# Optimization experiments

Measured on AMD Instinct MI355X. Metric: run time of the kernel, lower is better.

Reference implementation:

```python
import jax, jax.numpy as jnp
import numpy as np

N = 10000
E = 160000
IN_C = 512
OUT_C = 1024
NEG_SLOPE = 0.2


def setup_inputs() -> dict:
    key = jax.random.key(0)
    ks = jax.random.split(key, 12)
    x = jax.random.normal(ks[0], (N, IN_C), dtype=jnp.float32)
    edge_index = jax.random.randint(ks[1], (2, E), 0, N, dtype=jnp.int32)
    s_in = 1.0 / np.sqrt(IN_C)
    s_out = 1.0 / np.sqrt(OUT_C)
    return {
        "x": x,
        "edge_index": edge_index,
        "W1": jax.random.normal(ks[2], (IN_C, OUT_C), dtype=jnp.float32) * s_in,
        "a_src1": jax.random.normal(ks[3], (OUT_C,), dtype=jnp.float32) * s_out,
        "a_dst1": jax.random.normal(ks[4], (OUT_C,), dtype=jnp.float32) * s_out,
        "b1": jnp.zeros((OUT_C,), dtype=jnp.float32),
        "W2": jax.random.normal(ks[5], (IN_C, OUT_C), dtype=jnp.float32) * s_in,
        "a_src2": jax.random.normal(ks[6], (OUT_C,), dtype=jnp.float32) * s_out,
        "a_dst2": jax.random.normal(ks[7], (OUT_C,), dtype=jnp.float32) * s_out,
        "b2": jnp.zeros((OUT_C,), dtype=jnp.float32),
        "prelu_a": jnp.asarray(0.25, dtype=jnp.float32),
        "Wp1": jax.random.normal(ks[8], (OUT_C, OUT_C), dtype=jnp.float32) * s_out,
        "bp1": jnp.zeros((OUT_C,), dtype=jnp.float32),
        "Wp2": jax.random.normal(ks[9], (OUT_C, 1024), dtype=jnp.float32) * s_out,
    }


def _gat_conv(x, src, dst, W, a_src, a_dst, b):
    # x: [N, in], W: [in, out]. PyG GATConv, heads=1, self-loops already in src/dst.
    h = x @ W  # [N, out]
    alpha_s = h @ a_src  # [N]
    alpha_d = h @ a_dst  # [N]
    e = alpha_s[src] + alpha_d[dst]  # [E+N]
    e = jnp.where(e >= 0, e, NEG_SLOPE * e)  # LeakyReLU(0.2)
    # segment softmax over destination nodes
    m = jax.ops.segment_max(e, dst, num_segments=N)  # [N]
    ex = jnp.exp(e - m[dst])
    denom = jax.ops.segment_sum(ex, dst, num_segments=N)  # [N], >=1 via self-loops
    alpha = ex / denom[dst]  # [E+N]
    out = jax.ops.segment_sum(alpha[:, None] * h[src], dst, num_segments=N)
    return out + b


def reference(x, edge_index, W1, a_src1, a_dst1, b1, W2, a_src2, a_dst2, b2,
              prelu_a, Wp1, bp1, Wp2):
    # add self loops (PyG GATConv default)
    loops = jnp.arange(N, dtype=edge_index.dtype)
    src = jnp.concatenate([edge_index[0], loops])
    dst = jnp.concatenate([edge_index[1], loops])

    def prelu(v):
        return jnp.where(v >= 0, v, prelu_a * v)

    h1 = prelu(_gat_conv(x, src, dst, W1, a_src1, a_dst1, b1))  # [N, 1024]
    h2 = prelu(_gat_conv(x, src, dst, W2, a_src2, a_dst2, b2))  # [N, 1024]
    h = h1 + h2

    # semantic attention: project -> mean over nodes -> softmax over 1024 dims
    w = jnp.tanh(h @ Wp1 + bp1) @ Wp2  # [N, 1024]
    w = w.mean(axis=0)  # [1024]
    att = jax.nn.softmax(w, axis=0)  # [1024] == beta.mean(0).squeeze()
    return att * h1 + (1.0 - att) * h2
```

## Files before the change

### kernel.cpp

```cpp
#include <hip/hip_runtime.h>

#define IN_C 512
#define OUT_C 1024
#define NC2 2048
#define NEG_SLOPE 0.2f

typedef short frag8 __attribute__((ext_vector_type(8)));
typedef float f32x4 __attribute__((ext_vector_type(4)));

#define GLOAD_LDS16(g, l) __builtin_amdgcn_global_load_lds(\
    (const __attribute__((address_space(1))) void*)(g), \
    (__attribute__((address_space(3))) void*)(l), 16, 0, 0)

__device__ __forceinline__ unsigned short f2b(float f){
  unsigned u = __float_as_uint(f);
  unsigned r = (u + 0x7fffu + ((u >> 16) & 1u)) >> 16;
  return (unsigned short)r;
}
__device__ __forceinline__ unsigned encf(float f){
  unsigned u = __float_as_uint(f);
  return (u & 0x80000000u) ? ~u : (u | 0x80000000u);
}
__device__ __forceinline__ float decf(unsigned u){
  unsigned v = (u & 0x80000000u) ? (u & 0x7fffffffu) : ~u;
  return __uint_as_float(v);
}
__device__ __forceinline__ float leaky(float v){ return v >= 0.f ? v : NEG_SLOPE * v; }


__global__ void prep_kernel(const float* __restrict__ W1, const float* __restrict__ W2,
                            const float* __restrict__ Wp1,
                            const float* __restrict__ a_src1, const float* __restrict__ a_dst1,
                            const float* __restrict__ a_src2, const float* __restrict__ a_dst2,
                            unsigned short* __restrict__ WT, unsigned short* __restrict__ Wp1T,
                            float* __restrict__ uv){
  __shared__ float tile[32][33];
  int b = blockIdx.x;
  int tx = threadIdx.x & 31, ty = threadIdx.x >> 5;
  if (b < 1024){
    const float* in = (b >> 9) ? W2 : W1;
    int rowOff = (b >> 9) * OUT_C;
    int bb = b & 511;
    int c0 = (bb & 31) * 32, r0 = (bb >> 5) * 32;
    for (int i = ty; i < 32; i += 8)
      tile[i][tx] = in[(size_t)(r0 + i) * OUT_C + c0 + tx];
    __syncthreads();
    for (int i = ty; i < 32; i += 8)
      WT[(size_t)(c0 + i + rowOff) * IN_C + r0 + tx] = f2b(tile[tx][i]);
  } else if (b < 2048){
    int bb = b - 1024;
    int c0 = (bb & 31) * 32, r0 = (bb >> 5) * 32;
    for (int i = ty; i < 32; i += 8)
      tile[i][tx] = Wp1[(size_t)(r0 + i) * OUT_C + c0 + tx];
    __syncthreads();
    for (int i = ty; i < 32; i += 8)
      Wp1T[(size_t)(c0 + i) * OUT_C + r0 + tx] = f2b(tile[tx][i]);
  } else {
    int g = (b - 2048) * 4 + (threadIdx.x >> 6);
    int lane = threadIdx.x & 63;
    int which = g >> 9;
    int i = g & 511;
    const float* W = (which < 2) ? W1 : W2;
    const float* a = (which == 0) ? a_src1 : (which == 1) ? a_dst1 : (which == 2) ? a_src2 : a_dst2;
    const float* row = W + (size_t)i * OUT_C;
    float s = 0.f;
    for (int j = lane; j < OUT_C; j += 64) s += row[j] * a[j];
    for (int off = 32; off; off >>= 1) s += __shfl_down(s, off);
    if (lane == 0) uv[which * IN_C + i] = s;
  }
}


__global__ void alpha_kernel(const float* __restrict__ x, const float* __restrict__ uv,
                             unsigned short* __restrict__ xb,
                             float* __restrict__ as1, float* __restrict__ ad1,
                             float* __restrict__ as2, float* __restrict__ ad2,
                             float* __restrict__ self1, float* __restrict__ self2,
                             unsigned* __restrict__ m1e, unsigned* __restrict__ m2e,
                             int* counts, int* cursor, float* colsum, float* wv){
  int n = blockIdx.x;
  int w = threadIdx.x >> 6, lane = threadIdx.x & 63;
  __shared__ float sh[4];
  if (threadIdx.x == 0){ counts[n] = 0; cursor[n] = 0; }
  if (n < 8){
    int i = n * 256 + threadIdx.x;
    if (i < 1024) colsum[i] = 0.f; else wv[i - 1024] = 0.f;
  }
  const float* row = x + (size_t)n * IN_C;
  const float* u = uv + w * IN_C;
  float s = 0.f;
  for (int j = lane; j < IN_C; j += 64){
    float v = row[j];
    s += v * u[j];
    if (w == 0) xb[(size_t)n * IN_C + j] = f2b(v);
  }
  for (int off = 32; off; off >>= 1) s += __shfl_down(s, off);
  if (lane == 0){
    sh[w] = s;
    if (w == 0) as1[n] = s;
    else if (w == 1) ad1[n] = s;
    else if (w == 2) as2[n] = s;
    else ad2[n] = s;
  }
  __syncthreads();
  if (threadIdx.x == 0){
    float e1 = leaky(sh[0] + sh[1]);
    float e2 = leaky(sh[2] + sh[3]);
    self1[n] = e1; self2[n] = e2;
    m1e[n] = encf(e1); m2e[n] = encf(e2);
  }
}


__global__ void histmax_kernel(const int* __restrict__ src, const int* __restrict__ dst,
                               const float* __restrict__ as1, const float* __restrict__ ad1,
                               const float* __restrict__ as2, const float* __restrict__ ad2,
                               int* counts, unsigned* m1e, unsigned* m2e, int E){
  int e = blockIdx.x * 256 + threadIdx.x;
  if (e >= E) return;
  int s = src[e], d = dst[e];
  atomicAdd(&counts[d], 1);
  atomicMax(&m1e[d], encf(leaky(as1[s] + ad1[d])));
  atomicMax(&m2e[d], encf(leaky(as2[s] + ad2[d])));
}

__global__ void scanA_kernel(const int* __restrict__ counts, int* __restrict__ offs,
                             int* __restrict__ bsum, int n){
  __shared__ int wsum[4];
  int i = blockIdx.x * 256 + threadIdx.x;
  int wave = threadIdx.x >> 6, lane = threadIdx.x & 63;
  int v = (i < n) ? counts[i] : 0;
  int sc = v;
  for (int o = 1; o < 64; o <<= 1){
    int t = __shfl_up(sc, o);
    if (lane >= o) sc += t;
  }
  if (lane == 63) wsum[wave] = sc;
  __syncthreads();
  int wp = 0, tot = 0;
#pragma unroll
  for (int k = 0; k < 4; k++){
    int ws = wsum[k];
    if (k < wave) wp += ws;
    tot += ws;
  }
  if (i < n) offs[i] = wp + sc - v;
  if (threadIdx.x == 0) bsum[blockIdx.x] = tot;
}

__global__ void scanB_kernel(int* __restrict__ bsum, int nb){
  int lane = threadIdx.x;
  int v = (lane < nb) ? bsum[lane] : 0;
  int sc = v;
  for (int o = 1; o < 64; o <<= 1){
    int t = __shfl_up(sc, o);
    if (lane >= o) sc += t;
  }
  if (lane < nb) bsum[lane] = sc - v;
}

__global__ void scanC_kernel(int* __restrict__ offs, const int* __restrict__ bsum, int n){
  int i = blockIdx.x * 256 + threadIdx.x;
  if (i < n) offs[i] += bsum[blockIdx.x];
}

__global__ void denominit_kernel(const unsigned* __restrict__ m1e, const unsigned* __restrict__ m2e,
                                 const float* __restrict__ self1, const float* __restrict__ self2,
                                 float* __restrict__ m1, float* __restrict__ m2,
                                 float* __restrict__ den1, float* __restrict__ den2, int N){
  int i = blockIdx.x * 256 + threadIdx.x;
  if (i >= N) return;
  float a = decf(m1e[i]), b = decf(m2e[i]);
  m1[i] = a; m2[i] = b;
  den1[i] = expf(self1[i] - a);
  den2[i] = expf(self2[i] - b);
}

__global__ void scatterexp_kernel(const int* __restrict__ src, const int* __restrict__ dst,
                                  const int* __restrict__ offs, int* cursor,
                                  const float* __restrict__ as1, const float* __restrict__ ad1,
                                  const float* __restrict__ as2, const float* __restrict__ ad2,
                                  const float* __restrict__ m1, const float* __restrict__ m2,
                                  int* __restrict__ nsrc, float* __restrict__ nw1, float* __restrict__ nw2,
                                  float* den1, float* den2, int E){
  int e = blockIdx.x * 256 + threadIdx.x;
  if (e >= E) return;
  int s = src[e], d = dst[e];
  int p = atomicAdd(&cursor[d], 1);
  int idx = offs[d] + p;
  float x1 = expf(leaky(as1[s] + ad1[d]) - m1[d]);
  float x2 = expf(leaky(as2[s] + ad2[d]) - m2[d]);
  nsrc[idx] = s; nw1[idx] = x1; nw2[idx] = x2;
  atomicAdd(&den1[d], x1);
  atomicAdd(&den2[d], x2);
}


#define AGG_FMA8(ACC, W, U) \
  ACC[0] += (W) * __uint_as_float(((unsigned)(U).x) << 16); \
  ACC[1] += (W) * __uint_as_float(((unsigned)(U).x) & 0xffff0000u); \
  ACC[2] += (W) * __uint_as_float(((unsigned)(U).y) << 16); \
  ACC[3] += (W) * __uint_as_float(((unsigned)(U).y) & 0xffff0000u); \
  ACC[4] += (W) * __uint_as_float(((unsigned)(U).z) << 16); \
  ACC[5] += (W) * __uint_as_float(((unsigned)(U).z) & 0xffff0000u); \
  ACC[6] += (W) * __uint_as_float(((unsigned)(U).w) << 16); \
  ACC[7] += (W) * __uint_as_float(((unsigned)(U).w) & 0xffff0000u);

__global__ __launch_bounds__(256) void aggx_kernel(
    const int* __restrict__ counts, const int* __restrict__ offs,
    const int* __restrict__ nsrc, const float* __restrict__ nw1, const float* __restrict__ nw2,
    const float* __restrict__ den1, const float* __restrict__ den2,
    const float* __restrict__ self1, const float* __restrict__ self2,
    const float* __restrict__ m1, const float* __restrict__ m2,
    const unsigned short* __restrict__ xb,
    unsigned short* __restrict__ xa1b, unsigned short* __restrict__ xa2b, int N){
  int tid = threadIdx.x;
  int g = tid >> 4, hl = tid & 15;
  int grpbase = tid & 48;
  int d = blockIdx.y * 16 + g;
  if (d >= N) return;
  int colbase = blockIdx.x * 128 + hl * 8;
  float inv1 = 1.f / den1[d], inv2 = 1.f / den2[d];
  int deg = counts[d], off = offs[d];
  float acc1[8] = {0,0,0,0,0,0,0,0}, acc2[8] = {0,0,0,0,0,0,0,0};
  const unsigned short* Xb = xb + colbase;
  for (int base = 0; base < deg; base += 16){
    int i = base + hl;
    int s = 0; float w1 = 0.f, w2 = 0.f;
    if (i < deg){
      int p = off + i;
      s = nsrc[p];
      w1 = nw1[p] * inv1;
      w2 = nw2[p] * inv2;
    }
    int cnt = min(16, deg - base);
#pragma unroll 4
    for (int j = 0; j < cnt; j++){
      int sj = __shfl(s, grpbase + j);
      float w1j = __shfl(w1, grpbase + j);
      float w2j = __shfl(w2, grpbase + j);
      int4 u = *(const int4*)(Xb + (size_t)sj * IN_C);
      AGG_FMA8(acc1, w1j, u)
      AGG_FMA8(acc2, w2j, u)
    }
  }
  {
    float ws1 = expf(self1[d] - m1[d]) * inv1;
    float ws2 = expf(self2[d] - m2[d]) * inv2;
    int4 u = *(const int4*)(Xb + (size_t)d * IN_C);
    AGG_FMA8(acc1, ws1, u)
    AGG_FMA8(acc2, ws2, u)
  }
  size_t outb = (size_t)d * IN_C + colbase;
  int4 o1, o2;
  o1.x = (int)((unsigned)f2b(acc1[0]) | ((unsigned)f2b(acc1[1]) << 16));
  o1.y = (int)((unsigned)f2b(acc1[2]) | ((unsigned)f2b(acc1[3]) << 16));
  o1.z = (int)((unsigned)f2b(acc1[4]) | ((unsigned)f2b(acc1[5]) << 16));
  o1.w = (int)((unsigned)f2b(acc1[6]) | ((unsigned)f2b(acc1[7]) << 16));
  o2.x = (int)((unsigned)f2b(acc2[0]) | ((unsigned)f2b(acc2[1]) << 16));
  o2.y = (int)((unsigned)f2b(acc2[2]) | ((unsigned)f2b(acc2[3]) << 16));
  o2.z = (int)((unsigned)f2b(acc2[4]) | ((unsigned)f2b(acc2[5]) << 16));
  o2.w = (int)((unsigned)f2b(acc2[6]) | ((unsigned)f2b(acc2[7]) << 16));
  *(int4*)(xa1b + outb) = o1;
  *(int4*)(xa2b + outb) = o2;
}


__global__ __launch_bounds__(256) void gemmh_kernel(const unsigned short* __restrict__ A1,
                                                    const unsigned short* __restrict__ A2,
                                                    const unsigned short* __restrict__ BT,
                                                    const float* __restrict__ b1,
                                                    const float* __restrict__ b2,
                                                    const float* __restrict__ prelu_a,
                                                    unsigned short* __restrict__ hsum,
                                                    unsigned short* __restrict__ hdiff,
                                                    int M, int Mtiles, int perx){
  const int bid = blockIdx.x;
  const int xcd = bid & 7;
  const int li = bid >> 3;
  const int bn_t = li & 7;
  const int bm_t = xcd * perx + (li >> 3);
  if (bm_t >= Mtiles) return;
  const int bm = bm_t * 64, bn = bn_t * 128;
  __shared__ unsigned short Al[64 * 32];
  __shared__ unsigned short Bl[128 * 32];
  const int t = threadIdx.x;
  const int lane = t & 63, wid = t >> 6;
  const int wj = wid;
  const int l16 = lane & 15, q = lane >> 4;
  const int lch = (lane & 3) * 8;
  f32x4 acc1[4][2] = {};
  f32x4 acc2[4][2] = {};
  const int arow = bm + wid * 16 + (lane >> 2);
  const int brow0 = bn + wid * 32 + (lane >> 2);
  const int ga = min(arow, M - 1);
  const unsigned short* pa1 = A1 + (size_t)ga * IN_C + lch;
  const unsigned short* pa2 = A2 + (size_t)ga * IN_C + lch;
  const unsigned short* pb0 = BT + (size_t)brow0 * IN_C + lch;
  const unsigned short* pb1 = BT + (size_t)(brow0 + 16) * IN_C + lch;
  const size_t boff2 = (size_t)OUT_C * IN_C;
  for (int k0 = 0; k0 < IN_C; k0 += 32){
    GLOAD_LDS16(pa1 + k0, &Al[(wid * 16) * 32]);
    GLOAD_LDS16(pb0 + k0, &Bl[(wid * 32) * 32]);
    GLOAD_LDS16(pb1 + k0, &Bl[(wid * 32 + 16) * 32]);
    __syncthreads();
    frag8 af[4], bf[2];
#pragma unroll
    for (int mi = 0; mi < 4; mi++) af[mi] = *(const frag8*)&Al[(mi*16 + l16) * 32 + q*8];
#pragma unroll
    for (int nj = 0; nj < 2; nj++) bf[nj] = *(const frag8*)&Bl[(wj*32 + nj*16 + l16) * 32 + q*8];
#pragma unroll
    for (int mi = 0; mi < 4; mi++)
#pragma unroll
      for (int nj = 0; nj < 2; nj++)
        acc1[mi][nj] = __builtin_amdgcn_mfma_f32_16x16x32_bf16(af[mi], bf[nj], acc1[mi][nj], 0, 0, 0);
    __syncthreads();
  }
  for (int k0 = 0; k0 < IN_C; k0 += 32){
    GLOAD_LDS16(pa2 + k0, &Al[(wid * 16) * 32]);
    GLOAD_LDS16(pb0 + boff2 + k0, &Bl[(wid * 32) * 32]);
    GLOAD_LDS16(pb1 + boff2 + k0, &Bl[(wid * 32 + 16) * 32]);
    __syncthreads();
    frag8 af[4], bf[2];
#pragma unroll
    for (int mi = 0; mi < 4; mi++) af[mi] = *(const frag8*)&Al[(mi*16 + l16) * 32 + q*8];
#pragma unroll
    for (int nj = 0; nj < 2; nj++) bf[nj] = *(const frag8*)&Bl[(wj*32 + nj*16 + l16) * 32 + q*8];
#pragma unroll
    for (int mi = 0; mi < 4; mi++)
#pragma unroll
      for (int nj = 0; nj < 2; nj++)
        acc2[mi][nj] = __builtin_amdgcn_mfma_f32_16x16x32_bf16(af[mi], bf[nj], acc2[mi][nj], 0, 0, 0);
    __syncthreads();
  }
  float pa = prelu_a[0];
#pragma unroll
  for (int mi = 0; mi < 4; mi++){
#pragma unroll
    for (int r = 0; r < 4; r++){
      int row = bm + mi*16 + q*4 + r;
      if (row >= M) continue;
#pragma unroll
      for (int nj = 0; nj < 2; nj++){
        int col = bn + wj*32 + nj*16 + l16;
        float v1 = acc1[mi][nj][r] + b1[col];
        v1 = v1 >= 0.f ? v1 : pa * v1;
        float v2 = acc2[mi][nj][r] + b2[col];
        v2 = v2 >= 0.f ? v2 : pa * v2;
        size_t idx = (size_t)row * OUT_C + col;
        hsum[idx]  = f2b(v1 + v2);
        hdiff[idx] = f2b(v1 - v2);
      }
    }
  }
}


__global__ __launch_bounds__(256) void gemm2_kernel(const unsigned short* __restrict__ A,
                                                    const unsigned short* __restrict__ BT,
                                                    const float* __restrict__ bp1,
                                                    float* __restrict__ colsum,
                                                    int M, int Mtiles, int perx){
  const int bid = blockIdx.x;
  const int xcd = bid & 7;
  const int li = bid >> 3;
  const int bn_t = li & 7;
  const int bm_t = xcd * perx + (li >> 3);
  if (bm_t >= Mtiles) return;
  const int bm = bm_t * 64, bn = bn_t * 128;
  __shared__ unsigned short Al[64 * 32];
  __shared__ unsigned short Bl[128 * 32];
  __shared__ float cs[128];
  const int t = threadIdx.x;
  const int lane = t & 63, wid = t >> 6;
  const int wj = wid;
  const int l16 = lane & 15, q = lane >> 4;
  const int lch = (lane & 3) * 8;
  if (t < 128) cs[t] = 0.f;
  f32x4 acc[4][2] = {};
  const int arow = bm + wid * 16 + (lane >> 2);
  const int brow0 = bn + wid * 32 + (lane >> 2);
  const int ga = min(arow, M - 1);
  const unsigned short* pa = A + (size_t)ga * OUT_C + lch;
  const unsigned short* pb0 = BT + (size_t)brow0 * OUT_C + lch;
  const unsigned short* pb1 = BT + (size_t)(brow0 + 16) * OUT_C + lch;
  for (int k0 = 0; k0 < OUT_C; k0 += 32){
    GLOAD_LDS16(pa + k0, &Al[(wid * 16) * 32]);
    GLOAD_LDS16(pb0 + k0, &Bl[(wid * 32) * 32]);
    GLOAD_LDS16(pb1 + k0, &Bl[(wid * 32 + 16) * 32]);
    __syncthreads();
    frag8 af[4], bf[2];
#pragma unroll
    for (int mi = 0; mi < 4; mi++) af[mi] = *(const frag8*)&Al[(mi*16 + l16) * 32 + q*8];
#pragma unroll
    for (int nj = 0; nj < 2; nj++) bf[nj] = *(const frag8*)&Bl[(wj*32 + nj*16 + l16) * 32 + q*8];
#pragma unroll
    for (int mi = 0; mi < 4; mi++)
#pragma unroll
      for (int nj = 0; nj < 2; nj++)
        acc[mi][nj] = __builtin_amdgcn_mfma_f32_16x16x32_bf16(af[mi], bf[nj], acc[mi][nj], 0, 0, 0);
    __syncthreads();
  }
#pragma unroll
  for (int nj = 0; nj < 2; nj++){
    int col = bn + wj*32 + nj*16 + l16;
    float bias = bp1[col];
    float p = 0.f;
#pragma unroll
    for (int mi = 0; mi < 4; mi++){
#pragma unroll
      for (int r = 0; r < 4; r++){
        int row = bm + mi*16 + q*4 + r;
        float tv = tanhf(acc[mi][nj][r] + bias);
        if (row < M) p += tv;
      }
    }
    p += __shfl_xor(p, 16);
    p += __shfl_xor(p, 32);
    if (q == 0) atomicAdd(&cs[wj*32 + nj*16 + l16], p);
  }
  __syncthreads();
  if (t < 128) atomicAdd(&colsum[bn + t], cs[t]);
}


__global__ void wproj_kernel(const float* __restrict__ colsum, const float* __restrict__ Wp2,
                             float* __restrict__ wv){
  int o = blockIdx.x * 256 + threadIdx.x;
  int c0 = blockIdx.y * 128;
  float acc = 0.f;
  for (int c = c0; c < c0 + 128; c++) acc += colsum[c] * Wp2[(size_t)c * OUT_C + o];
  atomicAdd(&wv[o], acc);
}

__global__ __launch_bounds__(1024) void softmax_kernel(const float* __restrict__ wv,
                                                       float* __restrict__ att, float invN){
  int o = threadIdx.x;
  __shared__ float red[1024];
  float w = wv[o] * invN;
  red[o] = w; __syncthreads();
  for (int s = 512; s > 0; s >>= 1){ if (o < s) red[o] = fmaxf(red[o], red[o + s]); __syncthreads(); }
  float m = red[0]; __syncthreads();
  float e = expf(w - m);
  red[o] = e; __syncthreads();
  for (int s = 512; s > 0; s >>= 1){ if (o < s) red[o] += red[o + s]; __syncthreads(); }
  att[o] = e / red[0];
}

__global__ void combine_kernel(const float* __restrict__ att, const unsigned short* __restrict__ hs,
                               const unsigned short* __restrict__ hd, float* __restrict__ out, int total8){
  int i = blockIdx.x * 256 + threadIdx.x;
  if (i >= total8) return;
  int colb = (i & 127) * 8;
  int4 us = ((const int4*)hs)[i];
  int4 ud = ((const int4*)hd)[i];
  float4 a0 = *(const float4*)(att + colb);
  float4 a1 = *(const float4*)(att + colb + 4);
  float o[8]; float sv, dv;
  sv = __uint_as_float(((unsigned)us.x) << 16);        dv = __uint_as_float(((unsigned)ud.x) << 16);
  o[0] = 0.5f * sv + (a0.x - 0.5f) * dv;
  sv = __uint_as_float(((unsigned)us.x) & 0xffff0000u); dv = __uint_as_float(((unsigned)ud.x) & 0xffff0000u);
  o[1] = 0.5f * sv + (a0.y - 0.5f) * dv;
  sv = __uint_as_float(((unsigned)us.y) << 16);        dv = __uint_as_float(((unsigned)ud.y) << 16);
  o[2] = 0.5f * sv + (a0.z - 0.5f) * dv;
  sv = __uint_as_float(((unsigned)us.y) & 0xffff0000u); dv = __uint_as_float(((unsigned)ud.y) & 0xffff0000u);
  o[3] = 0.5f * sv + (a0.w - 0.5f) * dv;
  sv = __uint_as_float(((unsigned)us.z) << 16);        dv = __uint_as_float(((unsigned)ud.z) << 16);
  o[4] = 0.5f * sv + (a1.x - 0.5f) * dv;
  sv = __uint_as_float(((unsigned)us.z) & 0xffff0000u); dv = __uint_as_float(((unsigned)ud.z) & 0xffff0000u);
  o[5] = 0.5f * sv + (a1.y - 0.5f) * dv;
  sv = __uint_as_float(((unsigned)us.w) << 16);        dv = __uint_as_float(((unsigned)ud.w) << 16);
  o[6] = 0.5f * sv + (a1.z - 0.5f) * dv;
  sv = __uint_as_float(((unsigned)us.w) & 0xffff0000u); dv = __uint_as_float(((unsigned)ud.w) & 0xffff0000u);
  o[7] = 0.5f * sv + (a1.w - 0.5f) * dv;
  float4 f0; f0.x = o[0]; f0.y = o[1]; f0.z = o[2]; f0.w = o[3];
  float4 f1; f1.x = o[4]; f1.y = o[5]; f1.z = o[6]; f1.w = o[7];
  *(float4*)(out + (size_t)i * 8) = f0;
  *(float4*)(out + (size_t)i * 8 + 4) = f1;
}


extern "C" void kernel_launch(void* const* d_in, const int* in_sizes, int n_in,
                              void* d_out, int out_size, void* d_ws, size_t ws_size,
                              hipStream_t stream){
  const float* x      = (const float*)d_in[0];
  const int*   edge   = (const int*)d_in[1];
  const float* W1     = (const float*)d_in[2];
  const float* a_src1 = (const float*)d_in[3];
  const float* a_dst1 = (const float*)d_in[4];
  const float* b1     = (const float*)d_in[5];
  const float* W2     = (const float*)d_in[6];
  const float* a_src2 = (const float*)d_in[7];
  const float* a_dst2 = (const float*)d_in[8];
  const float* b2     = (const float*)d_in[9];
  const float* prelu_a= (const float*)d_in[10];
  const float* Wp1    = (const float*)d_in[11];
  const float* bp1    = (const float*)d_in[12];
  const float* Wp2    = (const float*)d_in[13];
  const int N = in_sizes[0] / IN_C;
  const int E = in_sizes[1] / 2;
  const int* srcArr = edge;
  const int* dstArr = edge + E;

  char* ws = (char*)d_ws;
  size_t o = 0;
  auto alloc = [&](size_t b) -> char* {
    char* p = ws + o;
    o = (o + b + 255) & ~(size_t)255;
    return p;
  };
  unsigned short* xb    = (unsigned short*)alloc((size_t)N * IN_C * 2);
  unsigned short* WT    = (unsigned short*)alloc((size_t)NC2 * IN_C * 2);
  unsigned short* Wp1T  = (unsigned short*)alloc((size_t)OUT_C * OUT_C * 2);
  unsigned short* xa1b  = (unsigned short*)alloc((size_t)N * IN_C * 2);
  unsigned short* xa2b  = (unsigned short*)alloc((size_t)N * IN_C * 2);
  unsigned short* hsum  = (unsigned short*)alloc((size_t)N * OUT_C * 2);
  unsigned short* hdiff = (unsigned short*)alloc((size_t)N * OUT_C * 2);
  float*          uv    = (float*)alloc(4 * IN_C * 4);
  float*          as1   = (float*)alloc((size_t)4 * N * 4);
  float* ad1 = as1 + N; float* as2 = as1 + 2 * N; float* ad2 = as1 + 3 * N;
  float*          self1 = (float*)alloc((size_t)2 * N * 4); float* self2 = self1 + N;
  unsigned*       m1e   = (unsigned*)alloc((size_t)2 * N * 4); unsigned* m2e = m1e + N;
  float*          m1    = (float*)alloc((size_t)2 * N * 4); float* m2 = m1 + N;
  float*          den1  = (float*)alloc((size_t)2 * N * 4); float* den2 = den1 + N;
  int*            counts= (int*)alloc((size_t)N * 4);
  int*            offs  = (int*)alloc((size_t)(N + 1) * 4);
  int*            cursor= (int*)alloc((size_t)N * 4);
  int*            bsum  = (int*)alloc(64 * 4);
  int*            nsrc  = (int*)alloc((size_t)E * 4);
  float*          nw1   = (float*)alloc((size_t)E * 4);
  float*          nw2   = (float*)alloc((size_t)E * 4);
  float*          colsum= (float*)alloc(OUT_C * 4);
  float*          wv    = (float*)alloc(OUT_C * 4);
  float*          att   = (float*)alloc(OUT_C * 4);

  const int Mtiles = (N + 63) / 64;
  const int perx = (Mtiles + 7) / 8;
  const int gemmgrid = 8 * perx * 8;
  const int nchunk = (N + 255) / 256;

  prep_kernel<<<2560, 256, 0, stream>>>(W1, W2, Wp1, a_src1, a_dst1, a_src2, a_dst2, WT, Wp1T, uv);
  alpha_kernel<<<N, 256, 0, stream>>>(x, uv, xb, as1, ad1, as2, ad2, self1, self2, m1e, m2e,
                                      counts, cursor, colsum, wv);
  histmax_kernel<<<(E + 255) / 256, 256, 0, stream>>>(srcArr, dstArr, as1, ad1, as2, ad2,
                                                      counts, m1e, m2e, E);
  scanA_kernel<<<nchunk, 256, 0, stream>>>(counts, offs, bsum, N);
  scanB_kernel<<<1, 64, 0, stream>>>(bsum, nchunk);
  scanC_kernel<<<nchunk, 256, 0, stream>>>(offs, bsum, N);
  denominit_kernel<<<nchunk, 256, 0, stream>>>(m1e, m2e, self1, self2, m1, m2, den1, den2, N);
  scatterexp_kernel<<<(E + 255) / 256, 256, 0, stream>>>(srcArr, dstArr, offs, cursor,
                                                         as1, ad1, as2, ad2, m1, m2,
                                                         nsrc, nw1, nw2, den1, den2, E);
  aggx_kernel<<<dim3(4, (N + 15) / 16), 256, 0, stream>>>(counts, offs, nsrc, nw1, nw2, den1, den2,
                                                          self1, self2, m1, m2, xb, xa1b, xa2b, N);
  gemmh_kernel<<<gemmgrid, 256, 0, stream>>>(xa1b, xa2b, WT, b1, b2, prelu_a,
                                             hsum, hdiff, N, Mtiles, perx);
  gemm2_kernel<<<gemmgrid, 256, 0, stream>>>(hsum, Wp1T, bp1, colsum, N, Mtiles, perx);
  wproj_kernel<<<dim3(4, 8), 256, 0, stream>>>(colsum, Wp2, wv);
  softmax_kernel<<<1, 1024, 0, stream>>>(wv, att, 1.0f / (float)N);
  combine_kernel<<<(N * OUT_C / 8 + 255) / 256, 256, 0, stream>>>(att, hsum, hdiff, (float*)d_out,
                                                                  N * OUT_C / 8);
}
```

Baseline: 325.0 us.

## Double-buffer LDS tiles and fuse dual-GEMM K loops in projection kernels

Both MFMA GEMM kernels now use double-buffered shared memory, so the async global-to-LDS loads for the next K slice are issued while the current slice is being computed. The head GEMM merges its two separate K loops (one per GAT branch) into a single loop that loads both A and B operands per step and interleaves the two accumulator chains. The second GEMM stages 64 K per step. The goal is to hide global load latency and halve the number of barriers. In exchange, shared memory per block grows about fourfold, which may reduce occupancy.

```diff
diff --git a/kernel.cpp b/kernel.cpp
--- a/kernel.cpp
+++ b/kernel.cpp
@@ -282,8 +282,8 @@
   const int bm_t = xcd * perx + (li >> 3);
   if (bm_t >= Mtiles) return;
   const int bm = bm_t * 64, bn = bn_t * 128;
-  __shared__ unsigned short Al[64 * 32];
-  __shared__ unsigned short Bl[128 * 32];
+  __shared__ unsigned short Al[2][2][64 * 32];
+  __shared__ unsigned short Bl[2][2][128 * 32];
   const int t = threadIdx.x;
   const int lane = t & 63, wid = t >> 6;
   const int wj = wid;
@@ -299,40 +299,54 @@
   const unsigned short* pb0 = BT + (size_t)brow0 * IN_C + lch;
   const unsigned short* pb1 = BT + (size_t)(brow0 + 16) * IN_C + lch;
   const size_t boff2 = (size_t)OUT_C * IN_C;
-  for (int k0 = 0; k0 < IN_C; k0 += 32){
-    GLOAD_LDS16(pa1 + k0, &Al[(wid * 16) * 32]);
-    GLOAD_LDS16(pb0 + k0, &Bl[(wid * 32) * 32]);
-    GLOAD_LDS16(pb1 + k0, &Bl[(wid * 32 + 16) * 32]);
+  const int aoff  = (wid * 16) * 32;
+  const int boffA = (wid * 32) * 32;
+  const int boffB = (wid * 32 + 16) * 32;
+
+#define STAGEH(B, k0) do { \
+    GLOAD_LDS16(pa1 + (k0), &Al[B][0][aoff]); \
+    GLOAD_LDS16(pa2 + (k0), &Al[B][1][aoff]); \
+    GLOAD_LDS16(pb0 + (k0), &Bl[B][0][boffA]); \
+    GLOAD_LDS16(pb1 + (k0), &Bl[B][0][boffB]); \
+    GLOAD_LDS16(pb0 + boff2 + (k0), &Bl[B][1][boffA]); \
+    GLOAD_LDS16(pb1 + boff2 + (k0), &Bl[B][1][boffB]); \
+  } while (0)
+
+#define COMPH(B) do { \
+    frag8 a1f[4], a2f[4], b1f[2], b2f[2]; \
+    _Pragma("unroll") \
+    for (int mi = 0; mi < 4; mi++){ \
+      a1f[mi] = *(const frag8*)&Al[B][0][(mi*16 + l16) * 32 + q*8]; \
+      a2f[mi] = *(const frag8*)&Al[B][1][(mi*16 + l16) * 32 + q*8]; \
+    } \
+    _Pragma("unroll") \
+    for (int nj = 0; nj < 2; nj++){ \
+      b1f[nj] = *(const frag8*)&Bl[B][0][(wj*32 + nj*16 + l16) * 32 + q*8]; \
+      b2f[nj] = *(const frag8*)&Bl[B][1][(wj*32 + nj*16 + l16) * 32 + q*8]; \
+    } \
+    _Pragma("unroll") \
+    for (int mi = 0; mi < 4; mi++) \
+      _Pragma("unroll") \
+      for (int nj = 0; nj < 2; nj++){ \
+        acc1[mi][nj] = __builtin_amdgcn_mfma_f32_16x16x32_bf16(a1f[mi], b1f[nj], acc1[mi][nj], 0, 0, 0); \
+        acc2[mi][nj] = __builtin_amdgcn_mfma_f32_16x16x32_bf16(a2f[mi], b2f[nj], acc2[mi][nj], 0, 0, 0); \
+      } \
+  } while (0)
+
+  STAGEH(0, 0);
+  __syncthreads();
+#pragma unroll 1
+  for (int it2 = 0; it2 < 8; ++it2){
+    STAGEH(1, (2*it2 + 1) * 32);
+    COMPH(0);
     __syncthreads();
-    frag8 af[4], bf[2];
-#pragma unroll
-    for (int mi = 0; mi < 4; mi++) af[mi] = *(const frag8*)&Al[(mi*16 + l16) * 32 + q*8];
-#pragma unroll
-    for (int nj = 0; nj < 2; nj++) bf[nj] = *(const frag8*)&Bl[(wj*32 + nj*16 + l16) * 32 + q*8];
-#pragma unroll
-    for (int mi = 0; mi < 4; mi++)
-#pragma unroll
-      for (int nj = 0; nj < 2; nj++)
-        acc1[mi][nj] = __builtin_amdgcn_mfma_f32_16x16x32_bf16(af[mi], bf[nj], acc1[mi][nj], 0, 0, 0);
+    if (it2 < 7) STAGEH(0, (2*it2 + 2) * 32);
+    COMPH(1);
     __syncthreads();
   }
-  for (int k0 = 0; k0 < IN_C; k0 += 32){
-    GLOAD_LDS16(pa2 + k0, &Al[(wid * 16) * 32]);
-    GLOAD_LDS16(pb0 + boff2 + k0, &Bl[(wid * 32) * 32]);
-    GLOAD_LDS16(pb1 + boff2 + k0, &Bl[(wid * 32 + 16) * 32]);
-    __syncthreads();
-    frag8 af[4], bf[2];
-#pragma unroll
-    for (int mi = 0; mi < 4; mi++) af[mi] = *(const frag8*)&Al[(mi*16 + l16) * 32 + q*8];
-#pragma unroll
-    for (int nj = 0; nj < 2; nj++) bf[nj] = *(const frag8*)&Bl[(wj*32 + nj*16 + l16) * 32 + q*8];
-#pragma unroll
-    for (int mi = 0; mi < 4; mi++)
-#pragma unroll
-      for (int nj = 0; nj < 2; nj++)
-        acc2[mi][nj] = __builtin_amdgcn_mfma_f32_16x16x32_bf16(af[mi], bf[nj], acc2[mi][nj], 0, 0, 0);
-    __syncthreads();
-  }
+#undef STAGEH
+#undef COMPH
+
   float pa = prelu_a[0];
 #pragma unroll
   for (int mi = 0; mi < 4; mi++){
@@ -368,8 +382,8 @@
   const int bm_t = xcd * perx + (li >> 3);
   if (bm_t >= Mtiles) return;
   const int bm = bm_t * 64, bn = bn_t * 128;
-  __shared__ unsigned short Al[64 * 32];
-  __shared__ unsigned short Bl[128 * 32];
+  __shared__ unsigned short Al[2][2][64 * 32];
+  __shared__ unsigned short Bl[2][2][128 * 32];
   __shared__ float cs[128];
   const int t = threadIdx.x;
   const int lane = t & 63, wid = t >> 6;
@@ -384,23 +398,57 @@
   const unsigned short* pa = A + (size_t)ga * OUT_C + lch;
   const unsigned short* pb0 = BT + (size_t)brow0 * OUT_C + lch;
   const unsigned short* pb1 = BT + (size_t)(brow0 + 16) * OUT_C + lch;
-  for (int k0 = 0; k0 < OUT_C; k0 += 32){
-    GLOAD_LDS16(pa + k0, &Al[(wid * 16) * 32]);
-    GLOAD_LDS16(pb0 + k0, &Bl[(wid * 32) * 32]);
-    GLOAD_LDS16(pb1 + k0, &Bl[(wid * 32 + 16) * 32]);
+  const int aoff  = (wid * 16) * 32;
+  const int boffA = (wid * 32) * 32;
+  const int boffB = (wid * 32 + 16) * 32;
+
+#define STAGE2(B, k0) do { \
+    GLOAD_LDS16(pa + (k0), &Al[B][0][aoff]); \
+    GLOAD_LDS16(pa + (k0) + 32, &Al[B][1][aoff]); \
+    GLOAD_LDS16(pb0 + (k0), &Bl[B][0][boffA]); \
+    GLOAD_LDS16(pb1 + (k0), &Bl[B][0][boffB]); \
+    GLOAD_LDS16(pb0 + (k0) + 32, &Bl[B][1][boffA]); \
+    GLOAD_LDS16(pb1 + (k0) + 32, &Bl[B][1][boffB]); \
+  } while (0)
+
+#define COMP2(B) do { \
+    frag8 af0[4], af1[4], bf0[2], bf1[2]; \
+    _Pragma("unroll") \
+    for (int mi = 0; mi < 4; mi++){ \
+      af0[mi] = *(const frag8*)&Al[B][0][(mi*16 + l16) * 32 + q*8]; \
+      af1[mi] = *(const frag8*)&Al[B][1][(mi*16 + l16) * 32 + q*8]; \
+    } \
+    _Pragma("unroll") \
+    for (int nj = 0; nj < 2; nj++){ \
+      bf0[nj] = *(const frag8*)&Bl[B][0][(wj*32 + nj*16 + l16) * 32 + q*8]; \
+      bf1[nj] = *(const frag8*)&Bl[B][1][(wj*32 + nj*16 + l16) * 32 + q*8]; \
+    } \
+    _Pragma("unroll") \
+    for (int mi = 0; mi < 4; mi++) \
+      _Pragma("unroll") \
+      for (int nj = 0; nj < 2; nj++) \
+        acc[mi][nj] = __builtin_amdgcn_mfma_f32_16x16x32_bf16(af0[mi], bf0[nj], acc[mi][nj], 0, 0, 0); \
+    _Pragma("unroll") \
+    for (int mi = 0; mi < 4; mi++) \
+      _Pragma("unroll") \
+      for (int nj = 0; nj < 2; nj++) \
+        acc[mi][nj] = __builtin_amdgcn_mfma_f32_16x16x32_bf16(af1[mi], bf1[nj], acc[mi][nj], 0, 0, 0); \
+  } while (0)
+
+  STAGE2(0, 0);
+  __syncthreads();
+#pragma unroll 1
+  for (int it2 = 0; it2 < 8; ++it2){
+    STAGE2(1, (2*it2 + 1) * 64);
+    COMP2(0);
     __syncthreads();
-    frag8 af[4], bf[2];
-#pragma unroll
-    for (int mi = 0; mi < 4; mi++) af[mi] = *(const frag8*)&Al[(mi*16 + l16) * 32 + q*8];
-#pragma unroll
-    for (int nj = 0; nj < 2; nj++) bf[nj] = *(const frag8*)&Bl[(wj*32 + nj*16 + l16) * 32 + q*8];
-#pragma unroll
-    for (int mi = 0; mi < 4; mi++)
-#pragma unroll
-      for (int nj = 0; nj < 2; nj++)
-        acc[mi][nj] = __builtin_amdgcn_mfma_f32_16x16x32_bf16(af[mi], bf[nj], acc[mi][nj], 0, 0, 0);
+    if (it2 < 7) STAGE2(0, (2*it2 + 2) * 64);
+    COMP2(1);
     __syncthreads();
   }
+#undef STAGE2
+#undef COMP2
+
 #pragma unroll
   for (int nj = 0; nj < 2; nj++){
     int col = bn + wj*32 + nj*16 + l16;
```

After: 329.5 us. Within noise of the previous version (+1.4%).

## Enlarge GEMM tiles to 128x128 with swizzled LDS and fused dual-GEMM loop

Applied to the files above, without the earlier changes.

Both MFMA GEMM kernels move from 64x128 block tiles to 128x128, with a 2x2 wave layout so each wave computes a 64x64 sub-tile. This raises operand reuse per LDS load. The two K-loops in gemmh are merged into one loop that stages both A and B pairs per step, halving the number of barriers. An XOR swizzle is applied to the LDS column chunks, matched on the load and fragment-read sides, to reduce bank conflicts. Output stores use nontemporal hints and launch_bounds requests 2 blocks per CU; the larger tiles raise register and LDS use and cut the block count, which may hurt occupancy and load balance.

```diff
diff --git a/kernel.cpp b/kernel.cpp
--- a/kernel.cpp
+++ b/kernel.cpp
@@ -7,6 +7,7 @@
 
 typedef short frag8 __attribute__((ext_vector_type(8)));
 typedef float f32x4 __attribute__((ext_vector_type(4)));
+typedef int i32x4 __attribute__((ext_vector_type(4)));
 
 #define GLOAD_LDS16(g, l) __builtin_amdgcn_global_load_lds(\
     (const __attribute__((address_space(1))) void*)(g), \
@@ -252,7 +253,7 @@
     AGG_FMA8(acc2, ws2, u)
   }
   size_t outb = (size_t)d * IN_C + colbase;
-  int4 o1, o2;
+  i32x4 o1, o2;
   o1.x = (int)((unsigned)f2b(acc1[0]) | ((unsigned)f2b(acc1[1]) << 16));
   o1.y = (int)((unsigned)f2b(acc1[2]) | ((unsigned)f2b(acc1[3]) << 16));
   o1.z = (int)((unsigned)f2b(acc1[4]) | ((unsigned)f2b(acc1[5]) << 16));
@@ -261,163 +262,180 @@
   o2.y = (int)((unsigned)f2b(acc2[2]) | ((unsigned)f2b(acc2[3]) << 16));
   o2.z = (int)((unsigned)f2b(acc2[4]) | ((unsigned)f2b(acc2[5]) << 16));
   o2.w = (int)((unsigned)f2b(acc2[6]) | ((unsigned)f2b(acc2[7]) << 16));
-  *(int4*)(xa1b + outb) = o1;
-  *(int4*)(xa2b + outb) = o2;
-}
-
-
-__global__ __launch_bounds__(256) void gemmh_kernel(const unsigned short* __restrict__ A1,
-                                                    const unsigned short* __restrict__ A2,
-                                                    const unsigned short* __restrict__ BT,
-                                                    const float* __restrict__ b1,
-                                                    const float* __restrict__ b2,
-                                                    const float* __restrict__ prelu_a,
-                                                    unsigned short* __restrict__ hsum,
-                                                    unsigned short* __restrict__ hdiff,
-                                                    int M, int Mtiles, int perx){
+  __builtin_nontemporal_store(o1, (i32x4*)(xa1b + outb));
+  __builtin_nontemporal_store(o2, (i32x4*)(xa2b + outb));
+}
+
+
+__global__ __launch_bounds__(256, 2) void gemmh_kernel(const unsigned short* __restrict__ A1,
+                                                       const unsigned short* __restrict__ A2,
+                                                       const unsigned short* __restrict__ BT,
+                                                       const float* __restrict__ b1,
+                                                       const float* __restrict__ b2,
+                                                       const float* __restrict__ prelu_a,
+                                                       unsigned short* __restrict__ hsum,
+                                                       unsigned short* __restrict__ hdiff,
+                                                       int M, int Mtiles, int perx){
   const int bid = blockIdx.x;
   const int xcd = bid & 7;
   const int li = bid >> 3;
   const int bn_t = li & 7;
   const int bm_t = xcd * perx + (li >> 3);
   if (bm_t >= Mtiles) return;
-  const int bm = bm_t * 64, bn = bn_t * 128;
-  __shared__ unsigned short Al[64 * 32];
-  __shared__ unsigned short Bl[128 * 32];
+  const int bm = bm_t * 128, bn = bn_t * 128;
+  __shared__ unsigned short Al[2][128 * 32];
+  __shared__ unsigned short Bl[2][128 * 32];
   const int t = threadIdx.x;
   const int lane = t & 63, wid = t >> 6;
-  const int wj = wid;
+  const int wr = wid >> 1, wc = wid & 1;
   const int l16 = lane & 15, q = lane >> 4;
-  const int lch = (lane & 3) * 8;
-  f32x4 acc1[4][2] = {};
-  f32x4 acc2[4][2] = {};
-  const int arow = bm + wid * 16 + (lane >> 2);
-  const int brow0 = bn + wid * 32 + (lane >> 2);
-  const int ga = min(arow, M - 1);
-  const unsigned short* pa1 = A1 + (size_t)ga * IN_C + lch;
-  const unsigned short* pa2 = A2 + (size_t)ga * IN_C + lch;
-  const unsigned short* pb0 = BT + (size_t)brow0 * IN_C + lch;
-  const unsigned short* pb1 = BT + (size_t)(brow0 + 16) * IN_C + lch;
-  const size_t boff2 = (size_t)OUT_C * IN_C;
+  const int qs = (q ^ ((l16 >> 1) & 3)) * 8;
+  const int lch = (((lane & 3) ^ ((lane >> 3) & 3)) * 8);
+  f32x4 acc1[4][4] = {};
+  f32x4 acc2[4][4] = {};
+  const int srow = wid * 32 + (lane >> 2);
+  const int ga0 = min(bm + srow, M - 1);
+  const int ga1 = min(bm + srow + 16, M - 1);
+  const unsigned short* pa1_0 = A1 + (size_t)ga0 * IN_C + lch;
+  const unsigned short* pa1_1 = A1 + (size_t)ga1 * IN_C + lch;
+  const unsigned short* pa2_0 = A2 + (size_t)ga0 * IN_C + lch;
+  const unsigned short* pa2_1 = A2 + (size_t)ga1 * IN_C + lch;
+  const unsigned short* pb1_0 = BT + (size_t)(bn + srow) * IN_C + lch;
+  const unsigned short* pb1_1 = BT + (size_t)(bn + srow + 16) * IN_C + lch;
+  const unsigned short* pb2_0 = pb1_0 + (size_t)OUT_C * IN_C;
+  const unsigned short* pb2_1 = pb1_1 + (size_t)OUT_C * IN_C;
+  const int so0 = (wid * 32) * 32;
+  const int so1 = (wid * 32 + 16) * 32;
+
   for (int k0 = 0; k0 < IN_C; k0 += 32){
-    GLOAD_LDS16(pa1 + k0, &Al[(wid * 16) * 32]);
-    GLOAD_LDS16(pb0 + k0, &Bl[(wid * 32) * 32]);
-    GLOAD_LDS16(pb1 + k0, &Bl[(wid * 32 + 16) * 32]);
+    GLOAD_LDS16(pa1_0 + k0, &Al[0][so0]);
+    GLOAD_LDS16(pa1_1 + k0, &Al[0][so1]);
+    GLOAD_LDS16(pa2_0 + k0, &Al[1][so0]);
+    GLOAD_LDS16(pa2_1 + k0, &Al[1][so1]);
+    GLOAD_LDS16(pb1_0 + k0, &Bl[0][so0]);
+    GLOAD_LDS16(pb1_1 + k0, &Bl[0][so1]);
+    GLOAD_LDS16(pb2_0 + k0, &Bl[1][so0]);
+    GLOAD_LDS16(pb2_1 + k0, &Bl[1][so1]);
     __syncthreads();
-    frag8 af[4], bf[2];
-#pragma unroll
-    for (int mi = 0; mi < 4; mi++) af[mi] = *(const frag8*)&Al[(mi*16 + l16) * 32 + q*8];
-#pragma unroll
-    for (int nj = 0; nj < 2; nj++) bf[nj] = *(const frag8*)&Bl[(wj*32 + nj*16 + l16) * 32 + q*8];
-#pragma unroll
-    for (int mi = 0; mi < 4; mi++)
-#pragma unroll
-      for (int nj = 0; nj < 2; nj++)
-        acc1[mi][nj] = __builtin_amdgcn_mfma_f32_16x16x32_bf16(af[mi], bf[nj], acc1[mi][nj], 0, 0, 0);
+    {
+      frag8 af[4], bf[4];
+#pragma unroll
+      for (int mi = 0; mi < 4; mi++) af[mi] = *(const frag8*)&Al[0][(wr*64 + mi*16 + l16) * 32 + qs];
+#pragma unroll
+      for (int nj = 0; nj < 4; nj++) bf[nj] = *(const frag8*)&Bl[0][(wc*64 + nj*16 + l16) * 32 + qs];
+#pragma unroll
+      for (int mi = 0; mi < 4; mi++)
+#pragma unroll
+        for (int nj = 0; nj < 4; nj++)
+          acc1[mi][nj] = __builtin_amdgcn_mfma_f32_16x16x32_bf16(af[mi], bf[nj], acc1[mi][nj], 0, 0, 0);
+    }
+    {
+      frag8 af[4], bf[4];
+#pragma unroll
+      for (int mi = 0; mi < 4; mi++) af[mi] = *(const frag8*)&Al[1][(wr*64 + mi*16 + l16) * 32 + qs];
+#pragma unroll
+      for (int nj = 0; nj < 4; nj++) bf[nj] = *(const frag8*)&Bl[1][(wc*64 + nj*16 + l16) * 32 + qs];
+#pragma unroll
+      for (int mi = 0; mi < 4; mi++)
+#pragma unroll
+        for (int nj = 0; nj < 4; nj++)
+          acc2[mi][nj] = __builtin_amdgcn_mfma_f32_16x16x32_bf16(af[mi], bf[nj], acc2[mi][nj], 0, 0, 0);
+    }
     __syncthreads();
   }
-  for (int k0 = 0; k0 < IN_C; k0 += 32){
-    GLOAD_LDS16(pa2 + k0, &Al[(wid * 16) * 32]);
-    GLOAD_LDS16(pb0 + boff2 + k0, &Bl[(wid * 32) * 32]);
-    GLOAD_LDS16(pb1 + boff2 + k0, &Bl[(wid * 32 + 16) * 32]);
-    __syncthreads();
-    frag8 af[4], bf[2];
-#pragma unroll
-    for (int mi = 0; mi < 4; mi++) af[mi] = *(const frag8*)&Al[(mi*16 + l16) * 32 + q*8];
-#pragma unroll
-    for (int nj = 0; nj < 2; nj++) bf[nj] = *(const frag8*)&Bl[(wj*32 + nj*16 + l16) * 32 + q*8];
-#pragma unroll
-    for (int mi = 0; mi < 4; mi++)
-#pragma unroll
-      for (int nj = 0; nj < 2; nj++)
-        acc2[mi][nj] = __builtin_amdgcn_mfma_f32_16x16x32_bf16(af[mi], bf[nj], acc2[mi][nj], 0, 0, 0);
-    __syncthreads();
-  }
+
   float pa = prelu_a[0];
 #pragma unroll
   for (int mi = 0; mi < 4; mi++){
 #pragma unroll
     for (int r = 0; r < 4; r++){
-      int row = bm + mi*16 + q*4 + r;
+      int row = bm + wr*64 + mi*16 + q*4 + r;
       if (row >= M) continue;
 #pragma unroll
-      for (int nj = 0; nj < 2; nj++){
-        int col = bn + wj*32 + nj*16 + l16;
+      for (int nj = 0; nj < 4; nj++){
+        int col = bn + wc*64 + nj*16 + l16;
         float v1 = acc1[mi][nj][r] + b1[col];
         v1 = v1 >= 0.f ? v1 : pa * v1;
         float v2 = acc2[mi][nj][r] + b2[col];
         v2 = v2 >= 0.f ? v2 : pa * v2;
         size_t idx = (size_t)row * OUT_C + col;
-        hsum[idx]  = f2b(v1 + v2);
-        hdiff[idx] = f2b(v1 - v2);
+        __builtin_nontemporal_store(f2b(v1 + v2), &hsum[idx]);
+        __builtin_nontemporal_store(f2b(v1 - v2), &hdiff[idx]);
       }
     }
   }
 }
 
 
-__global__ __launch_bounds__(256) void gemm2_kernel(const unsigned short* __restrict__ A,
-                                                    const unsigned short* __restrict__ BT,
-                                                    const float* __restrict__ bp1,
-                                                    float* __restrict__ colsum,
-                                                    int M, int Mtiles, int perx){
+__global__ __launch_bounds__(256, 2) void gemm2_kernel(const unsigned short* __restrict__ A,
+                                                       const unsigned short* __restrict__ BT,
+                                                       const float* __restrict__ bp1,
+                                                       float* __restrict__ colsum,
+                                                       int M, int Mtiles, int perx){
   const int bid = blockIdx.x;
   const int xcd = bid & 7;
   const int li = bid >> 3;
   const int bn_t = li & 7;
   const int bm_t = xcd * perx + (li >> 3);
   if (bm_t >= Mtiles) return;
-  const int bm = bm_t * 64, bn = bn_t * 128;
-  __shared__ unsigned short Al[64 * 32];
+  const int bm = bm_t * 128, bn = bn_t * 128;
+  __shared__ unsigned short Al[128 * 32];
   __shared__ unsigned short Bl[128 * 32];
   __shared__ float cs[128];
   const int t = threadIdx.x;
   const int lane = t & 63, wid = t >> 6;
-  const int wj = wid;
+  const int wr = wid >> 1, wc = wid & 1;
   const int l16 = lane & 15, q = lane >> 4;
-  const int lch = (lane & 3) * 8;
+  const int qs = (q ^ ((l16 >> 1) & 3)) * 8;
+  const int lch = (((lane & 3) ^ ((lane >> 3) & 3)) * 8);
   if (t < 128) cs[t] = 0.f;
-  f32x4 acc[4][2] = {};
-  const int arow = bm + wid * 16 + (lane >> 2);
-  const int brow0 = bn + wid * 32 + (lane >> 2);
-  const int ga = min(arow, M - 1);
-  const unsigned short* pa = A + (size_t)ga * OUT_C + lch;
-  const unsigned short* pb0 = BT + (size_t)brow0 * OUT_C + lch;
-  const unsigned short* pb1 = BT + (size_t)(brow0 + 16) * OUT_C + lch;
+  f32x4 acc[4][4] = {};
+  const int srow = wid * 32 + (lane >> 2);
+  const int ga0 = min(bm + srow, M - 1);
+  const int ga1 = min(bm + srow + 16, M - 1);
+  const unsigned short* pa_0 = A + (size_t)ga0 * OUT_C + lch;
+  const unsigned short* pa_1 = A + (size_t)ga1 * OUT_C + lch;
+  const unsigned short* pb_0 = BT + (size_t)(bn + srow) * OUT_C + lch;
+  const unsigned short* pb_1 = BT + (size_t)(bn + srow + 16) * OUT_C + lch;
+  const int so0 = (wid * 32) * 32;
+  const int so1 = (wid * 32 + 16) * 32;
+
   for (int k0 = 0; k0 < OUT_C; k0 += 32){
-    GLOAD_LDS16(pa + k0, &Al[(wid * 16) * 32]);
-    GLOAD_LDS16(pb0 + k0, &Bl[(wid * 32) * 32]);
-    GLOAD_LDS16(pb1 + k0, &Bl[(wid * 32 + 16) * 32]);
+    GLOAD_LDS16(pa_0 + k0, &Al[so0]);
+    GLOAD_LDS16(pa_1 + k0, &Al[so1]);
+    GLOAD_LDS16(pb_0 + k0, &Bl[so0]);
+    GLOAD_LDS16(pb_1 + k0, &Bl[so1]);
     __syncthreads();
-    frag8 af[4], bf[2];
-#pragma unroll
-    for (int mi = 0; mi < 4; mi++) af[mi] = *(const frag8*)&Al[(mi*16 + l16) * 32 + q*8];
-#pragma unroll
-    for (int nj = 0; nj < 2; nj++) bf[nj] = *(const frag8*)&Bl[(wj*32 + nj*16 + l16) * 32 + q*8];
+    frag8 af[4], bf[4];
+#pragma unroll
+    for (int mi = 0; mi < 4; mi++) af[mi] = *(const frag8*)&Al[(wr*64 + mi*16 + l16) * 32 + qs];
+#pragma unroll
+    for (int nj = 0; nj < 4; nj++) bf[nj] = *(const frag8*)&Bl[(wc*64 + nj*16 + l16) * 32 + qs];
 #pragma unroll
     for (int mi = 0; mi < 4; mi++)
 #pragma unroll
-      for (int nj = 0; nj < 2; nj++)
+      for (int nj = 0; nj < 4; nj++)
         acc[mi][nj] = __builtin_amdgcn_mfma_f32_16x16x32_bf16(af[mi], bf[nj], acc[mi][nj], 0, 0, 0);
     __syncthreads();
   }
-#pragma unroll
-  for (int nj = 0; nj < 2; nj++){
-    int col = bn + wj*32 + nj*16 + l16;
+
+#pragma unroll
+  for (int nj = 0; nj < 4; nj++){
+    int col = bn + wc*64 + nj*16 + l16;
     float bias = bp1[col];
     float p = 0.f;
 #pragma unroll
     for (int mi = 0; mi < 4; mi++){
 #pragma unroll
       for (int r = 0; r < 4; r++){
-        int row = bm + mi*16 + q*4 + r;
+        int row = bm + wr*64 + mi*16 + q*4 + r;
         float tv = tanhf(acc[mi][nj][r] + bias);
         if (row < M) p += tv;
       }
     }
     p += __shfl_xor(p, 16);
     p += __shfl_xor(p, 32);
-    if (q == 0) atomicAdd(&cs[wj*32 + nj*16 + l16], p);
+    if (q == 0) atomicAdd(&cs[wc*64 + nj*16 + l16], p);
   }
   __syncthreads();
   if (t < 128) atomicAdd(&colsum[bn + t], cs[t]);
@@ -473,10 +491,10 @@
   o[6] = 0.5f * sv + (a1.z - 0.5f) * dv;
   sv = __uint_as_float(((unsigned)us.w) & 0xffff0000u); dv = __uint_as_float(((unsigned)ud.w) & 0xffff0000u);
   o[7] = 0.5f * sv + (a1.w - 0.5f) * dv;
-  float4 f0; f0.x = o[0]; f0.y = o[1]; f0.z = o[2]; f0.w = o[3];
-  float4 f1; f1.x = o[4]; f1.y = o[5]; f1.z = o[6]; f1.w = o[7];
-  *(float4*)(out + (size_t)i * 8) = f0;
-  *(float4*)(out + (size_t)i * 8 + 4) = f1;
+  f32x4 f0; f0[0] = o[0]; f0[1] = o[1]; f0[2] = o[2]; f0[3] = o[3];
+  f32x4 f1; f1[0] = o[4]; f1[1] = o[5]; f1[2] = o[6]; f1[3] = o[7];
+  __builtin_nontemporal_store(f0, (f32x4*)(out + (size_t)i * 8));
+  __builtin_nontemporal_store(f1, (f32x4*)(out + (size_t)i * 8 + 4));
 }
 
 
@@ -534,7 +552,7 @@
   float*          wv    = (float*)alloc(OUT_C * 4);
   float*          att   = (float*)alloc(OUT_C * 4);
 
-  const int Mtiles = (N + 63) / 64;
+  const int Mtiles = (N + 127) / 128;
   const int perx = (Mtiles + 7) / 8;
   const int gemmgrid = 8 * perx * 8;
   const int nchunk = (N + 255) / 256;
```

Result: slower. 339.3 us (+4.4%).
